# Optimization experiments

Hardware: AMD Instinct MI355X
Metric: run time of the kernel (lower is better)

## Reference

```python
import jax, jax.numpy as jnp
import numpy as np

# Constants derived from init_kwargs / input shapes
B = 4          # number of graphs (equal-sized point clouds)
N = 16384      # points per graph
STRIDE = 4     # center_sampler: strided sampling, ratio 0.25 -> M = N/4
K = 20         # k nearest neighbors
N_SCAL = 16    # reps '16x0+16x1': 16 scalars
N_VEC = 16     # 16 vectors (3 coeffs each)
D = N_SCAL + 3 * N_VEC   # 64 feature coeffs
HID = 128
OUT = 128


def transform_coeffs(x, R):
    """TensorReps('16x0+16x1') coefficient transform: scalars unchanged,
    each 3-vector v -> R @ v.  x: [n, D], R: [n, 3, 3]."""
    s = x[:, :N_SCAL]
    v = x[:, N_SCAL:].reshape(-1, N_VEC, 3)
    v = jnp.einsum('nab,nkb->nka', R, v)
    return jnp.concatenate([s, v.reshape(-1, 3 * N_VEC)], axis=-1)


def setup_inputs() -> dict:
    key = jax.random.key(0)
    ks = jax.random.split(key, 6)
    Ntot = B * N
    x = jax.random.normal(ks[0], (Ntot, D), jnp.float32)
    pos = jax.random.normal(ks[1], (Ntot, 3), jnp.float32)
    # orthonormal local frames via QR of random 3x3 matrices
    lf = jax.random.normal(ks[2], (Ntot, 3, 3), jnp.float32)
    lframes, _ = jnp.linalg.qr(lf)
    batch = jnp.repeat(jnp.arange(B, dtype=jnp.int32), N)
    W1 = jax.random.normal(ks[3], (2 * D, HID), jnp.float32) / np.sqrt(2 * D)
    b1 = jnp.zeros((HID,), jnp.float32)
    W2 = jax.random.normal(ks[4], (HID, OUT), jnp.float32) / np.sqrt(HID)
    b2 = jnp.zeros((OUT,), jnp.float32)
    return {"x": x, "pos": pos, "lframes": lframes, "batch": batch,
            "W1": W1, "b1": b1, "W2": W2, "b2": b2}


def reference(x, pos, lframes, batch, W1, b1, W2, b2):
    M = N // STRIDE
    # --- center_sampler: strided sampling per graph (CustomPointSampler) ---
    idx = (jnp.arange(B)[:, None] * N + jnp.arange(0, N, STRIDE)[None, :]).reshape(-1)  # [B*M]

    # --- transform features to global frame: coeffs with lframes^T ---
    kf = transform_coeffs(x, jnp.swapaxes(lframes, -1, -2))
    # --- concat_pos_to_features (transform_pos=False) ---
    kf = jnp.concatenate([kf, pos], axis=-1)            # [Ntot, 67]
    Dk = kf.shape[-1]

    # --- brute-force per-graph kNN: centers query against all nodes ---
    kf_b = kf.reshape(B, N, Dk)
    q = kf_b[:, ::STRIDE]                               # [B, M, Dk] centers
    d2 = (jnp.sum(q * q, -1)[:, :, None]
          + jnp.sum(kf_b * kf_b, -1)[:, None, :]
          - 2.0 * jnp.einsum('bmd,bnd->bmn', q, kf_b))  # [B, M, N]
    _, nbr = jax.lax.top_k(-d2, K)                      # [B, M, K] per-graph idx
    src = nbr + (jnp.arange(B) * N)[:, None, None]      # global node idx

    # --- gather dst/src node data ---
    x_dst = x[idx].reshape(B, M, D)
    lf_dst = lframes[idx]                               # [B*M, 3, 3]
    x_src = x[src.reshape(-1)].reshape(B, M, K, D)

    # --- EdgeConv (tensor-frames flavor): relative features rotated into the
    #     destination local frame, MLP over [x_i, R_i (x_j - x_i)], max-aggr ---
    rel = x_src - x_dst[:, :, None]                     # [B, M, K, D]
    R_edge = jnp.repeat(lf_dst, K, axis=0)              # [B*M*K, 3, 3]
    rel_local = transform_coeffs(rel.reshape(-1, D), R_edge).reshape(B, M, K, D)
    h = jnp.concatenate(
        [jnp.broadcast_to(x_dst[:, :, None], rel.shape), rel_local], axis=-1)  # [B,M,K,2D]
    msg = jax.nn.relu(h @ W1 + b1) @ W2 + b2            # [B, M, K, OUT]
    out = jnp.max(msg, axis=2).reshape(B * M, OUT)

    return out, pos[idx], batch[idx], lf_dst
```

## Files before the change

### kernel.cpp

```cpp
#include <hip/hip_runtime.h>
#include <hip/hip_bf16.h>

#define NTOT 65536
#define KNN  20
#define KROW 104

typedef __attribute__((ext_vector_type(4))) float f32x4;
typedef __attribute__((ext_vector_type(8))) short s16x8;

#define WS_NORM 13631488
#define WS_NBR  13893632
#define WS_WT1  15204352
#define WS_WT2  15237120

#define ROWS 144
#define CSTR 257
#define OFF_TAUG 149056
#define OFF_MG   149312
#define KNN_SMEM 157504
#define THRESH 64

__device__ __forceinline__ unsigned short f2bf_rne(float v){
  unsigned u = __float_as_uint(v);
  return (unsigned short)((u + 0x7FFFu + ((u >> 16) & 1u)) >> 16);
}

__global__ __launch_bounds__(256) void k_prep(const float* __restrict__ x,
        const float* __restrict__ pos, const float* __restrict__ lfr,
        unsigned short* __restrict__ kfB, float* __restrict__ normB){
  int n = blockIdx.x * 256 + threadIdx.x;
  const float* xr = x + n * 64;
  float R[9];
  #pragma unroll
  for (int j = 0; j < 9; j++) R[j] = lfr[n * 9 + j];
  float c[67];
  #pragma unroll
  for (int i = 0; i < 16; i++) c[i] = xr[i];
  #pragma unroll
  for (int k = 0; k < 16; k++){
    float v0 = xr[16 + 3*k], v1 = xr[17 + 3*k], v2 = xr[18 + 3*k];
    #pragma unroll
    for (int a = 0; a < 3; a++)
      c[16 + 3*k + a] = R[a] * v0 + R[3 + a] * v1 + R[6 + a] * v2;
  }
  #pragma unroll
  for (int a = 0; a < 3; a++) c[64 + a] = pos[n * 3 + a];
  float sq = 0.f;
  #pragma unroll
  for (int d = 0; d < 67; d++) sq += c[d] * c[d];
  __attribute__((aligned(16))) unsigned short row[KROW];
  #pragma unroll
  for (int d = 0; d < 67; d++) row[d] = f2bf_rne(c[d]);
  #pragma unroll
  for (int d = 67; d < KROW; d++) row[d] = 0;
  uint4* dst = (uint4*)(kfB + (size_t)n * KROW);
  const uint4* s4 = (const uint4*)row;
  #pragma unroll
  for (int i = 0; i < 13; i++) dst[i] = s4[i];
  normB[n] = sq;
}

__global__ __launch_bounds__(256) void k_wprep(const float* __restrict__ W1,
        const float* __restrict__ W2, unsigned short* __restrict__ wb1,
        unsigned short* __restrict__ wb2){
  int a = blockIdx.x * 256 + threadIdx.x;
  int kb = a >> 12, n = (a >> 5) & 127, kl = a & 31;
  int i = ((kb << 5) + kl) * 128 + n;
  wb1[a] = f2bf_rne(W1[i]);
  wb2[a] = f2bf_rne(W2[i]);
}

__device__ __forceinline__ unsigned col_compact(unsigned* buf,
    int col, int cn, int lane){
  unsigned e0 = (lane < cn) ? buf[lane * CSTR + col] : 0xFFFFFFFFu;
  unsigned e1 = (lane + 64 < cn) ? buf[(lane + 64) * CSTR + col] : 0xFFFFFFFFu;
  unsigned T = 0;
  #pragma unroll 1
  for (int b = 31; b >= 0; --b){
    unsigned cand = T | (1u << b);
    int c = __popcll(__ballot(e0 < cand)) + __popcll(__ballot(e1 < cand));
    if (c <= 31) T = cand;
  }
  unsigned long long m0 = __ballot(e0 <= T);
  unsigned long long m1 = __ballot(e1 <= T);
  int b1 = __popcll(m0);
  unsigned long long ltm = (1ull << lane) - 1ull;
  if (e0 <= T) buf[__popcll(m0 & ltm) * CSTR + col] = e0;
  if (e1 <= T) buf[(b1 + __popcll(m1 & ltm)) * CSTR + col] = e1;
  return T;
}

__global__ __launch_bounds__(1024, 4) void k_knn(
    const unsigned short* __restrict__ kfB, const float* __restrict__ normB,
    const float* __restrict__ x, const float* __restrict__ pos,
    const float* __restrict__ lfr, int* __restrict__ nbr){
  __shared__ __attribute__((aligned(16))) char smem[KNN_SMEM];
  unsigned* buf = (unsigned*)smem;
  unsigned* tauG = (unsigned*)(smem + OFF_TAUG);
  unsigned* mg = (unsigned*)(smem + OFF_MG);

  int tid = threadIdx.x;
  int blk = blockIdx.x;
  int b = blk & 3;
  int qloc0 = (blk >> 2) << 6;
  int bbase = b << 14;

  if (tid < 64) tauG[tid] = 0x7F7FC000u;

  int lane = tid & 63;
  int wv = tid >> 6;
  int wq = wv >> 2;
  int kq = wv & 3;
  int l15 = lane & 15, quad = lane >> 4;
  int colB = (wq << 6) + kq;

  int qloc = qloc0 + (wq << 4);
  s16x8 af[3];
  {
    int nodeA = bbase + ((qloc + l15) << 2);
    const unsigned short* ap = kfB + (size_t)nodeA * KROW + quad * 8;
    af[0] = *(const s16x8*)(ap);
    af[1] = *(const s16x8*)(ap + 32);
    af[2] = *(const s16x8*)(ap + 64);
  }
  float qsq[4];
  #pragma unroll
  for (int r = 0; r < 4; r++)
    qsq[r] = normB[bbase + ((qloc + (quad << 2) + r) << 2)];

  float tauR[4] = {3.0e38f, 3.0e38f, 3.0e38f, 3.0e38f};
  int cntR[4];

  const unsigned short* kp = kfB + (size_t)(bbase + (kq << 12) + l15) * KROW + quad * 8;
  const float* np = normB + (bbase + (kq << 12) + l15);

  __syncthreads();

  s16x8 cK[4][3];
  float nK[4];
  #define LOADK(S) do { \
      cK[S][0] = *(const s16x8*)(kp); \
      cK[S][1] = *(const s16x8*)(kp + 32); \
      cK[S][2] = *(const s16x8*)(kp + 64); \
      nK[S] = *np; kp += 16 * KROW; np += 16; } while (0)

  auto comp = [&](const s16x8 bf[3], float ksqv, float d2v[4]){
    f32x4 acc = (f32x4){0.f, 0.f, 0.f, 0.f};
    acc = __builtin_amdgcn_mfma_f32_16x16x32_bf16(af[0], bf[0], acc, 0, 0, 0);
    acc = __builtin_amdgcn_mfma_f32_16x16x32_bf16(af[1], bf[1], acc, 0, 0, 0);
    acc = __builtin_amdgcn_mfma_f32_16x16x32_bf16(af[2], bf[2], acc, 0, 0, 0);
    #pragma unroll
    for (int r = 0; r < 4; r++)
      d2v[r] = fmaxf(qsq[r] + ksqv - 2.f * acc[r], 0.f);
  };

  auto seed = [&](const float d2v[4], int g){
    int kidx = (kq << 12) + (g << 4) + l15;
    #pragma unroll
    for (int r = 0; r < 4; r++){
      unsigned pk = ((__float_as_uint(d2v[r]) + 0x2000u) & 0xFFFFC000u) | (unsigned)kidx;
      buf[((g << 4) + l15) * CSTR + colB + (quad << 4) + (r << 2)] = pk;
    }
  };

  auto process = [&](const float d2v[4], int g){
    bool p[4];
    #pragma unroll
    for (int r = 0; r < 4; r++) p[r] = d2v[r] < tauR[r];
    if (__any(p[0] | p[1] | p[2] | p[3])){
      int kidx = (kq << 12) + (g << 4) + l15;
      #pragma unroll
      for (int r = 0; r < 4; r++){
        unsigned long long m = __ballot(p[r]);
        if (m){
          int lo = (int)((m >> (quad << 4)) & 0xFFFFull);
          if (lo){
            int colr = colB + (quad << 4) + (r << 2);
            int pre = __popc(lo & ((1 << l15) - 1));
            if (p[r]){
              unsigned pk = ((__float_as_uint(d2v[r]) + 0x2000u) & 0xFFFFC000u) | (unsigned)kidx;
              buf[(cntR[r] + pre) * CSTR + colr] = pk;
            }
            cntR[r] += __popc(lo);
          }
        }
      }
    }
  };

  auto check_compact = [&](int limit){
    #pragma unroll
    for (int r = 0; r < 4; r++){
      unsigned long long mr = __ballot(cntR[r] > limit);
      while (mr){
        int ldr = __ffsll((unsigned long long)mr) - 1;
        int qd = ldr >> 4;
        mr &= ~(0xFFFFull << (qd << 4));
        int col = colB + (qd << 4) + (r << 2);
        int cn = __shfl(cntR[r], qd << 4, 64);
        unsigned T = col_compact(buf, col, cn, lane);
        if (quad == qd) cntR[r] = 32;
        if (lane == 0) atomicMin(&tauG[(wq << 4) + (qd << 2) + r], T);
      }
    }
  };

  float d2v[4];
  LOADK(0); LOADK(1); LOADK(2); LOADK(3);
  #pragma unroll
  for (int j = 0; j < 4; j++){
    comp(cK[j], nK[j], d2v);
    seed(d2v, j);
    LOADK(j);
  }
  #pragma unroll
  for (int r = 0; r < 4; r++) cntR[r] = 64;

  #pragma unroll 1
  for (int g = 4; g < 256; g += 4){
    #pragma unroll
    for (int j = 0; j < 4; j++){
      comp(cK[j], nK[j], d2v);
      LOADK(j);
      process(d2v, g + j);
    }
    check_compact(THRESH);
    uint4 tg = *(const uint4*)&tauG[(wq << 4) + (quad << 2)];
    tauR[0] = __uint_as_float(tg.x & 0xFFFFC000u);
    tauR[1] = __uint_as_float(tg.y & 0xFFFFC000u);
    tauR[2] = __uint_as_float(tg.z & 0xFFFFC000u);
    tauR[3] = __uint_as_float(tg.w & 0xFFFFC000u);
  }

  check_compact(32);
  __syncthreads();

  #pragma unroll 1
  for (int s = 0; s < 4; s++){
    int q = (wv << 2) + s;
    unsigned e0 = buf[(lane & 31) * CSTR + (q << 2) + (lane >> 5)];
    unsigned e1 = buf[(lane & 31) * CSTR + (q << 2) + 2 + (lane >> 5)];
    unsigned T = 0;
    #pragma unroll 1
    for (int bb = 31; bb >= 0; --bb){
      unsigned cand = T | (1u << bb);
      int c = __popcll(__ballot(e0 < cand)) + __popcll(__ballot(e1 < cand));
      if (c <= 31) T = cand;
    }
    unsigned long long m0 = __ballot(e0 <= T);
    unsigned long long m1 = __ballot(e1 <= T);
    int b1 = __popcll(m0);
    unsigned long long ltm = (1ull << lane) - 1ull;
    int p0 = __popcll(m0 & ltm);
    int p1 = b1 + __popcll(m1 & ltm);
    if ((e0 <= T) && (p0 < 32)) mg[(q << 5) + p0] = e0;
    if ((e1 <= T) && (p1 < 32)) mg[(q << 5) + p1] = e1;
  }
  __syncthreads();

  double* qkf = (double*)(smem);
  double* rrD = (double*)(smem + 34304);
  int*    rrI = (int*)(smem + 50688);

  {
    int t16 = tid & 15, q = tid >> 4;
    int node = bbase + ((qloc0 + q) << 2);
    const float* xr = x + node * 64;
    for (int dd = t16; dd < 67; dd += 16){
      double val;
      if (dd < 16) val = (double)xr[dd];
      else if (dd < 64){
        int r = dd - 16; int k = r / 3; int a = r - 3 * k;
        val = (double)lfr[node*9 + a]     * (double)xr[16 + 3*k]
            + (double)lfr[node*9 + 3 + a] * (double)xr[17 + 3*k]
            + (double)lfr[node*9 + 6 + a] * (double)xr[18 + 3*k];
      } else val = (double)pos[node*3 + (dd - 64)];
      qkf[q * 67 + dd] = val;
    }
  }
  __syncthreads();
  {
    int t16 = tid & 15, q = tid >> 4;
    for (int j = t16; j < 32; j += 16){
      int idx = (int)(mg[(q << 5) + j] & 0x3FFFu);
      int node = bbase + idx;
      const float* xr = x + node * 64;
      double R[9];
      #pragma unroll
      for (int t = 0; t < 9; t++) R[t] = (double)lfr[node * 9 + t];
      double d2 = 0.0;
      #pragma unroll
      for (int dd = 0; dd < 16; dd++){ double t = (double)xr[dd] - qkf[q*67 + dd]; d2 += t * t; }
      #pragma unroll
      for (int k = 0; k < 16; k++){
        double v0 = xr[16 + 3*k], v1 = xr[17 + 3*k], v2 = xr[18 + 3*k];
        #pragma unroll
        for (int a = 0; a < 3; a++){
          double val = R[a] * v0 + R[3 + a] * v1 + R[6 + a] * v2;
          double t = val - qkf[q*67 + 16 + 3*k + a]; d2 += t * t;
        }
      }
      #pragma unroll
      for (int a = 0; a < 3; a++){ double t = (double)pos[node*3 + a] - qkf[q*67 + 64 + a]; d2 += t * t; }
      rrD[q * 32 + j] = d2; rrI[q * 32 + j] = idx;
    }
  }
  __syncthreads();
  if (tid < 64){
    int qq = tid;
    int qid = (b << 12) + qloc0 + qq;
    #pragma unroll 1
    for (int s = 0; s < KNN; s++){
      double best = rrD[qq * 32 + s]; int bi = s;
      for (int t = s + 1; t < 32; t++){
        double v = rrD[qq * 32 + t]; if (v < best){ best = v; bi = t; }
      }
      double tv = rrD[qq * 32 + bi]; rrD[qq * 32 + bi] = rrD[qq * 32 + s]; rrD[qq * 32 + s] = tv;
      int ti = rrI[qq * 32 + bi]; rrI[qq * 32 + bi] = rrI[qq * 32 + s]; rrI[qq * 32 + s] = ti;
      nbr[qid * KNN + s] = bbase + rrI[qq * 32 + s];
    }
  }
}

#define M_X   0
#define M_H   43520
#define M_W1  84480
#define M_W2  117248
#define M_B1  150016
#define M_B2  150528
#define M_NBR 151040
#define M_XD  151680
#define M_LF  153728
#define M_SZ  154048

__global__ __launch_bounds__(512) void k_mlp(const float* __restrict__ x,
    const float* __restrict__ lfr, const int* __restrict__ nbr,
    const unsigned short* __restrict__ wb1, const unsigned short* __restrict__ wb2,
    const float* __restrict__ b1, const float* __restrict__ b2,
    float* __restrict__ out){
  __shared__ __attribute__((aligned(16))) char smem[M_SZ];
  float* xsF = (float*)(smem + M_X);
  unsigned short* a1B = (unsigned short*)(smem + M_X);
  unsigned short* hB = (unsigned short*)(smem + M_H);
  unsigned short* wt1 = (unsigned short*)(smem + M_W1);
  unsigned short* wt2 = (unsigned short*)(smem + M_W2);
  float* b1L = (float*)(smem + M_B1);
  float* b2L = (float*)(smem + M_B2);
  int*   nbrL = (int*)(smem + M_NBR);
  float* xdL  = (float*)(smem + M_XD);
  float* lfL  = (float*)(smem + M_LF);

  int tid = threadIdx.x;
  int qid0 = blockIdx.x * 8;
  int lane = tid & 63, wv = tid >> 6;
  int l15 = lane & 15, quad = lane >> 4;

  {
    const uint4* g1 = (const uint4*)wb1;
    const uint4* g2 = (const uint4*)wb2;
    uint4* l1 = (uint4*)wt1;
    uint4* l2 = (uint4*)wt2;
    #pragma unroll
    for (int p = 0; p < 4; p++){
      l1[tid + (p << 9)] = g1[tid + (p << 9)];
      l2[tid + (p << 9)] = g2[tid + (p << 9)];
    }
  }
  if (tid < 160) nbrL[tid] = nbr[qid0 * 20 + tid];
  {
    int q = tid >> 6, d = tid & 63;
    int qid = qid0 + q;
    int node = ((qid >> 12) << 14) + ((qid & 4095) << 2);
    xdL[q * 64 + d] = x[node * 64 + d];
  }
  if (tid < 72){
    int q = tid / 9, j = tid - 9 * q;
    int qid = qid0 + q;
    int node = ((qid >> 12) << 14) + ((qid & 4095) << 2);
    lfL[q * 9 + j] = lfr[node * 9 + j];
  }
  if (tid < 128){ b1L[tid] = b1[tid]; b2L[tid] = b2[tid]; }
  __syncthreads();

  {
    int f4 = tid & 15;
    #pragma unroll
    for (int p = 0; p < 5; p++){
      int e = (tid >> 4) + (p << 5);
      float4 v = *(const float4*)&x[(size_t)nbrL[e] * 64 + (f4 << 2)];
      *(float4*)&xsF[e * 68 + (f4 << 2)] = v;
    }
  }
  __syncthreads();

  {
    int d = tid & 127, eo = tid >> 7;
    int cls, kk = 0, aa = 0;
    if (d < 64) cls = 0;
    else { int dd = d - 64;
      if (dd < 16) cls = 1;
      else { cls = 2; int r = dd - 16; kk = (r * 21846) >> 16; aa = r - 3 * kk; } }
    int hoff = ((d >> 5) * 160) * 32 + (d & 31);
    #pragma unroll 4
    for (int p = 0; p < 40; p++){
      int e = eo + (p << 2);
      int q = (e * 3277) >> 16;
      float v;
      if (cls == 0) v = xdL[q * 64 + d];
      else if (cls == 1) v = xsF[e * 68 + (d - 64)] - xdL[q * 64 + (d - 64)];
      else {
        int base = 16 + 3 * kk;
        float u0 = xsF[e * 68 + base]     - xdL[q * 64 + base];
        float u1 = xsF[e * 68 + base + 1] - xdL[q * 64 + base + 1];
        float u2 = xsF[e * 68 + base + 2] - xdL[q * 64 + base + 2];
        v = lfL[q * 9 + aa * 3] * u0 + lfL[q * 9 + aa * 3 + 1] * u1 + lfL[q * 9 + aa * 3 + 2] * u2;
      }
      hB[hoff + e * 32] = f2bf_rne(v);
    }
  }
  __syncthreads();

  {
    s16x8 bfr[4];
    #pragma unroll
    for (int ks = 0; ks < 4; ks++)
      bfr[ks] = *(const s16x8*)(wt1 + ((ks * 128 + (wv << 4) + l15) * 32 + (quad << 3)));
    float b1v = b1L[(wv << 4) + l15];
    int colhi = wv >> 1, collo = ((wv & 1) << 4) + l15;
    #pragma unroll
    for (int mt = 0; mt < 10; mt++){
      f32x4 acc = (f32x4){0.f, 0.f, 0.f, 0.f};
      #pragma unroll
      for (int ks = 0; ks < 4; ks++){
        s16x8 af = *(const s16x8*)(hB + ((ks * 160 + (mt << 4) + l15) * 32 + (quad << 3)));
        acc = __builtin_amdgcn_mfma_f32_16x16x32_bf16(af, bfr[ks], acc, 0, 0, 0);
      }
      #pragma unroll
      for (int r = 0; r < 4; r++){
        float v = fmaxf(acc[r] + b1v, 0.f);
        int row = (mt << 4) + (quad << 2) + r;
        a1B[(colhi * 160 + row) * 32 + collo] = f2bf_rne(v);
      }
    }
  }
  __syncthreads();

  {
    s16x8 bfr[4];
    #pragma unroll
    for (int ks = 0; ks < 4; ks++)
      bfr[ks] = *(const s16x8*)(wt2 + ((ks * 128 + (wv << 4) + l15) * 32 + (quad << 3)));
    float mxv[8];
    #pragma unroll
    for (int q = 0; q < 8; q++) mxv[q] = -3.0e38f;
    const int QA[10]  = {0,0,1,2,3,4,4,5,6,7};
    const int CUT[10] = {16,4,8,12,16,16,4,8,12,16};
    #pragma unroll
    for (int mt = 0; mt < 10; mt++){
      f32x4 acc = (f32x4){0.f, 0.f, 0.f, 0.f};
      #pragma unroll
      for (int ks = 0; ks < 4; ks++){
        s16x8 af = *(const s16x8*)(a1B + ((ks * 160 + (mt << 4) + l15) * 32 + (quad << 3)));
        acc = __builtin_amdgcn_mfma_f32_16x16x32_bf16(af, bfr[ks], acc, 0, 0, 0);
      }
      int qa = QA[mt], cut = CUT[mt];
      if (cut >= 16){
        #pragma unroll
        for (int r = 0; r < 4; r++) mxv[qa] = fmaxf(mxv[qa], acc[r]);
      } else {
        #pragma unroll
        for (int r = 0; r < 4; r++){
          int lr = (quad << 2) + r;
          bool toA = lr < cut;
          mxv[qa]     = fmaxf(mxv[qa],     toA ? acc[r] : -3.0e38f);
          mxv[qa + 1] = fmaxf(mxv[qa + 1], toA ? -3.0e38f : acc[r]);
        }
      }
    }
    #pragma unroll
    for (int q = 0; q < 8; q++){
      float v = mxv[q];
      v = fmaxf(v, __shfl_xor(v, 16, 64));
      v = fmaxf(v, __shfl_xor(v, 32, 64));
      mxv[q] = v;
    }
    if (quad == 0){
      int col = (wv << 4) + l15;
      float b2v = b2L[col];
      #pragma unroll
      for (int q = 0; q < 8; q++)
        out[(size_t)(qid0 + q) * 128 + col] = mxv[q] + b2v;
    }
  }
}

__global__ __launch_bounds__(256) void k_tail(const float* __restrict__ pos,
    const float* __restrict__ lfr, float* __restrict__ out){
  int q = blockIdx.x * 256 + threadIdx.x;
  int b = q >> 12;
  int node = (b << 14) + ((q & 4095) << 2);
  float* o_pos = out + 2097152;
  float* o_bat = out + 2146304;
  float* o_lf  = out + 2162688;
  #pragma unroll
  for (int j = 0; j < 3; j++) o_pos[q * 3 + j] = pos[node * 3 + j];
  o_bat[q] = (float)b;
  #pragma unroll
  for (int j = 0; j < 9; j++) o_lf[q * 9 + j] = lfr[node * 9 + j];
}

extern "C" void kernel_launch(void* const* d_in, const int* in_sizes, int n_in,
                              void* d_out, int out_size, void* d_ws, size_t ws_size,
                              hipStream_t stream){
  const float* x   = (const float*)d_in[0];
  const float* pos = (const float*)d_in[1];
  const float* lfr = (const float*)d_in[2];
  const float* W1  = (const float*)d_in[4];
  const float* b1  = (const float*)d_in[5];
  const float* W2  = (const float*)d_in[6];
  const float* b2  = (const float*)d_in[7];

  unsigned short* kfB = (unsigned short*)d_ws;
  float* normB = (float*)((char*)d_ws + WS_NORM);
  int*   nbr   = (int*)((char*)d_ws + WS_NBR);
  unsigned short* wb1 = (unsigned short*)((char*)d_ws + WS_WT1);
  unsigned short* wb2 = (unsigned short*)((char*)d_ws + WS_WT2);
  float* out = (float*)d_out;

  hipLaunchKernelGGL(k_prep,  dim3(256),  dim3(256), 0, stream, x, pos, lfr, kfB, normB);
  hipLaunchKernelGGL(k_wprep, dim3(64),   dim3(256), 0, stream, W1, W2, wb1, wb2);
  hipLaunchKernelGGL(k_knn,   dim3(256),  dim3(1024), 0, stream, kfB, normB, x, pos, lfr, nbr);
  hipLaunchKernelGGL(k_mlp,   dim3(2048), dim3(512), 0, stream, x, lfr, nbr, wb1, wb2, b1, b2, out);
  hipLaunchKernelGGL(k_tail,  dim3(64),   dim3(256), 0, stream, pos, lfr, out);
}
```

Before: 604.1 us.

## Split kNN fp64 rerank into separate kernel with parallel rank-based selection

Moves the fp64 exact re-ranking of the 32 candidate neighbors out of the kNN kernel into a new kernel with one thread per candidate. Candidates pass through global memory as 16-bit indices. The serial selection sort over 32 entries, run by 64 threads, is replaced by a shuffle-based rank count. This frees the tail of the 1024-thread kNN kernel, which previously had mostly idle threads, and shrinks its shared memory. The cost is an extra launch and a global round trip for the candidate lists.

```diff
diff --git a/kernel.cpp b/kernel.cpp
--- a/kernel.cpp
+++ b/kernel.cpp
@@ -12,12 +12,12 @@
 #define WS_NBR  13893632
 #define WS_WT1  15204352
 #define WS_WT2  15237120
+#define WS_MG   15269888
 
 #define ROWS 144
 #define CSTR 257
 #define OFF_TAUG 149056
-#define OFF_MG   149312
-#define KNN_SMEM 157504
+#define KNN_SMEM 149312
 #define THRESH 64
 
 __device__ __forceinline__ unsigned short f2bf_rne(float v){
@@ -92,12 +92,10 @@
 
 __global__ __launch_bounds__(1024, 4) void k_knn(
     const unsigned short* __restrict__ kfB, const float* __restrict__ normB,
-    const float* __restrict__ x, const float* __restrict__ pos,
-    const float* __restrict__ lfr, int* __restrict__ nbr){
+    unsigned short* __restrict__ mgG){
   __shared__ __attribute__((aligned(16))) char smem[KNN_SMEM];
   unsigned* buf = (unsigned*)smem;
   unsigned* tauG = (unsigned*)(smem + OFF_TAUG);
-  unsigned* mg = (unsigned*)(smem + OFF_MG);
 
   int tid = threadIdx.x;
   int blk = blockIdx.x;
@@ -238,6 +236,7 @@
   #pragma unroll 1
   for (int s = 0; s < 4; s++){
     int q = (wv << 2) + s;
+    int qid = (b << 12) + qloc0 + q;
     unsigned e0 = buf[(lane & 31) * CSTR + (q << 2) + (lane >> 5)];
     unsigned e1 = buf[(lane & 31) * CSTR + (q << 2) + 2 + (lane >> 5)];
     unsigned T = 0;
@@ -253,73 +252,68 @@
     unsigned long long ltm = (1ull << lane) - 1ull;
     int p0 = __popcll(m0 & ltm);
     int p1 = b1 + __popcll(m1 & ltm);
-    if ((e0 <= T) && (p0 < 32)) mg[(q << 5) + p0] = e0;
-    if ((e1 <= T) && (p1 < 32)) mg[(q << 5) + p1] = e1;
-  }
-  __syncthreads();
-
-  double* qkf = (double*)(smem);
-  double* rrD = (double*)(smem + 34304);
-  int*    rrI = (int*)(smem + 50688);
-
-  {
-    int t16 = tid & 15, q = tid >> 4;
-    int node = bbase + ((qloc0 + q) << 2);
-    const float* xr = x + node * 64;
-    for (int dd = t16; dd < 67; dd += 16){
+    if ((e0 <= T) && (p0 < 32)) mgG[qid * 32 + p0] = (unsigned short)(e0 & 0x3FFFu);
+    if ((e1 <= T) && (p1 < 32)) mgG[qid * 32 + p1] = (unsigned short)(e1 & 0x3FFFu);
+  }
+}
+
+__global__ __launch_bounds__(256) void k_rerank(const float* __restrict__ x,
+    const float* __restrict__ pos, const float* __restrict__ lfr,
+    const unsigned short* __restrict__ mgG, int* __restrict__ nbr){
+  __shared__ double qkf[8][68];
+  int tid = threadIdx.x;
+  int ql = tid >> 5;
+  int j  = tid & 31;
+  int qid = blockIdx.x * 8 + ql;
+  int b = qid >> 12;
+  int bbase = b << 14;
+  int node_q = bbase + ((qid & 4095) << 2);
+
+  {
+    const float* xr = x + node_q * 64;
+    for (int dd = j; dd < 67; dd += 32){
       double val;
       if (dd < 16) val = (double)xr[dd];
       else if (dd < 64){
         int r = dd - 16; int k = r / 3; int a = r - 3 * k;
-        val = (double)lfr[node*9 + a]     * (double)xr[16 + 3*k]
-            + (double)lfr[node*9 + 3 + a] * (double)xr[17 + 3*k]
-            + (double)lfr[node*9 + 6 + a] * (double)xr[18 + 3*k];
-      } else val = (double)pos[node*3 + (dd - 64)];
-      qkf[q * 67 + dd] = val;
-    }
-  }
-  __syncthreads();
-  {
-    int t16 = tid & 15, q = tid >> 4;
-    for (int j = t16; j < 32; j += 16){
-      int idx = (int)(mg[(q << 5) + j] & 0x3FFFu);
-      int node = bbase + idx;
-      const float* xr = x + node * 64;
-      double R[9];
-      #pragma unroll
-      for (int t = 0; t < 9; t++) R[t] = (double)lfr[node * 9 + t];
-      double d2 = 0.0;
-      #pragma unroll
-      for (int dd = 0; dd < 16; dd++){ double t = (double)xr[dd] - qkf[q*67 + dd]; d2 += t * t; }
-      #pragma unroll
-      for (int k = 0; k < 16; k++){
-        double v0 = xr[16 + 3*k], v1 = xr[17 + 3*k], v2 = xr[18 + 3*k];
-        #pragma unroll
-        for (int a = 0; a < 3; a++){
-          double val = R[a] * v0 + R[3 + a] * v1 + R[6 + a] * v2;
-          double t = val - qkf[q*67 + 16 + 3*k + a]; d2 += t * t;
-        }
-      }
-      #pragma unroll
-      for (int a = 0; a < 3; a++){ double t = (double)pos[node*3 + a] - qkf[q*67 + 64 + a]; d2 += t * t; }
-      rrD[q * 32 + j] = d2; rrI[q * 32 + j] = idx;
-    }
-  }
-  __syncthreads();
-  if (tid < 64){
-    int qq = tid;
-    int qid = (b << 12) + qloc0 + qq;
-    #pragma unroll 1
-    for (int s = 0; s < KNN; s++){
-      double best = rrD[qq * 32 + s]; int bi = s;
-      for (int t = s + 1; t < 32; t++){
-        double v = rrD[qq * 32 + t]; if (v < best){ best = v; bi = t; }
-      }
-      double tv = rrD[qq * 32 + bi]; rrD[qq * 32 + bi] = rrD[qq * 32 + s]; rrD[qq * 32 + s] = tv;
-      int ti = rrI[qq * 32 + bi]; rrI[qq * 32 + bi] = rrI[qq * 32 + s]; rrI[qq * 32 + s] = ti;
-      nbr[qid * KNN + s] = bbase + rrI[qq * 32 + s];
-    }
-  }
+        val = (double)lfr[node_q*9 + a]     * (double)xr[16 + 3*k]
+            + (double)lfr[node_q*9 + 3 + a] * (double)xr[17 + 3*k]
+            + (double)lfr[node_q*9 + 6 + a] * (double)xr[18 + 3*k];
+      } else val = (double)pos[node_q*3 + (dd - 64)];
+      qkf[ql][dd] = val;
+    }
+  }
+  __syncthreads();
+
+  int idx = (int)mgG[qid * 32 + j];
+  int node = bbase + idx;
+  const float* xr = x + node * 64;
+  double R[9];
+  #pragma unroll
+  for (int t = 0; t < 9; t++) R[t] = (double)lfr[node * 9 + t];
+  double d2 = 0.0;
+  #pragma unroll
+  for (int dd = 0; dd < 16; dd++){ double t = (double)xr[dd] - qkf[ql][dd]; d2 += t * t; }
+  #pragma unroll
+  for (int k = 0; k < 16; k++){
+    double v0 = xr[16 + 3*k], v1 = xr[17 + 3*k], v2 = xr[18 + 3*k];
+    #pragma unroll
+    for (int a = 0; a < 3; a++){
+      double val = R[a] * v0 + R[3 + a] * v1 + R[6 + a] * v2;
+      double t = val - qkf[ql][16 + 3*k + a]; d2 += t * t;
+    }
+  }
+  #pragma unroll
+  for (int a = 0; a < 3; a++){ double t = (double)pos[node*3 + a] - qkf[ql][64 + a]; d2 += t * t; }
+
+  int base = (tid & 32) ? 32 : 0;
+  int rank = 0;
+  #pragma unroll 1
+  for (int j2 = 0; j2 < 32; j2++){
+    double o = __shfl(d2, base + j2, 64);
+    rank += (o < d2) || ((o == d2) && (j2 < j));
+  }
+  if (rank < KNN) nbr[qid * KNN + rank] = node;
 }
 
 #define M_X   0
@@ -525,11 +519,13 @@
   int*   nbr   = (int*)((char*)d_ws + WS_NBR);
   unsigned short* wb1 = (unsigned short*)((char*)d_ws + WS_WT1);
   unsigned short* wb2 = (unsigned short*)((char*)d_ws + WS_WT2);
+  unsigned short* mgG = (unsigned short*)((char*)d_ws + WS_MG);
   float* out = (float*)d_out;
 
-  hipLaunchKernelGGL(k_prep,  dim3(256),  dim3(256), 0, stream, x, pos, lfr, kfB, normB);
-  hipLaunchKernelGGL(k_wprep, dim3(64),   dim3(256), 0, stream, W1, W2, wb1, wb2);
-  hipLaunchKernelGGL(k_knn,   dim3(256),  dim3(1024), 0, stream, kfB, normB, x, pos, lfr, nbr);
-  hipLaunchKernelGGL(k_mlp,   dim3(2048), dim3(512), 0, stream, x, lfr, nbr, wb1, wb2, b1, b2, out);
-  hipLaunchKernelGGL(k_tail,  dim3(64),   dim3(256), 0, stream, pos, lfr, out);
-}
+  hipLaunchKernelGGL(k_prep,   dim3(256),  dim3(256),  0, stream, x, pos, lfr, kfB, normB);
+  hipLaunchKernelGGL(k_wprep,  dim3(64),   dim3(256),  0, stream, W1, W2, wb1, wb2);
+  hipLaunchKernelGGL(k_knn,    dim3(256),  dim3(1024), 0, stream, kfB, normB, mgG);
+  hipLaunchKernelGGL(k_rerank, dim3(2048), dim3(256),  0, stream, x, pos, lfr, mgG, nbr);
+  hipLaunchKernelGGL(k_mlp,    dim3(2048), dim3(512),  0, stream, x, lfr, nbr, wb1, wb2, b1, b2, out);
+  hipLaunchKernelGGL(k_tail,   dim3(64),   dim3(256),  0, stream, pos, lfr, out);
+}
```

Measured after the change: 597.4 us. Within noise of the previous version (-1.1%).
